# Kernel optimization log

Measured on AMD Instinct MI355X. Metric: run time of the kernel, lower is better.

## Reference

```python
import jax, jax.numpy as jnp
import numpy as np

N = 50000      # nodes
E = 800000     # edges (before self-loops)
DIN = 256      # node_feature_dim
H = 3          # attention heads
C = 64         # hidden channels per head
DOUT = 16      # output_dim
NEG_SLOPE = 0.2


def setup_inputs() -> dict:
    key = jax.random.key(0)
    ks = jax.random.split(key, 12)
    s = 0.05
    return {
        "x": jax.random.normal(ks[0], (N, DIN), dtype=jnp.float32),
        "W1": jax.random.normal(ks[1], (DIN, H * C), dtype=jnp.float32) * s,
        "att_src1": jax.random.normal(ks[2], (H, C), dtype=jnp.float32) * s,
        "att_dst1": jax.random.normal(ks[3], (H, C), dtype=jnp.float32) * s,
        "b1": jnp.zeros((C,), dtype=jnp.float32),
        "W2": jax.random.normal(ks[4], (C, H * C), dtype=jnp.float32) * s,
        "att_src2": jax.random.normal(ks[5], (H, C), dtype=jnp.float32) * s,
        "att_dst2": jax.random.normal(ks[6], (H, C), dtype=jnp.float32) * s,
        "b2": jnp.zeros((C,), dtype=jnp.float32),
        "Wl": jax.random.normal(ks[7], (C, DOUT), dtype=jnp.float32) * s,
        "bl": jnp.zeros((DOUT,), dtype=jnp.float32),
        "edge_index": jax.random.randint(ks[8], (2, E), 0, N, dtype=jnp.int64),
    }


def _gat_layer(x, src, dst, W, att_src, att_dst, bias):
    """PyG GATConv, concat=False (mean over heads), self-loops already in src/dst."""
    n = x.shape[0]
    xw = (x @ W).reshape(n, H, C)                       # [N,H,C]
    a_src = jnp.sum(xw * att_src, axis=-1)              # [N,H]
    a_dst = jnp.sum(xw * att_dst, axis=-1)              # [N,H]
    alpha = jax.nn.leaky_relu(a_src[src] + a_dst[dst], NEG_SLOPE)  # [Etot,H]
    # segment softmax over incoming edges of each dst node
    m = jax.ops.segment_max(alpha, dst, num_segments=n)            # [N,H]
    e = jnp.exp(alpha - m[dst])
    ssum = jax.ops.segment_sum(e, dst, num_segments=n)             # [N,H]
    coef = e / (ssum[dst] + 1e-16)                                 # [Etot,H]
    out = jax.ops.segment_sum(xw[src] * coef[:, :, None], dst, num_segments=n)  # [N,H,C]
    return out.mean(axis=1) + bias                      # [N,C]


def reference(x, W1, att_src1, att_dst1, b1, W2, att_src2, att_dst2, b2, Wl, bl, edge_index):
    n = x.shape[0]
    loops = jnp.arange(n, dtype=edge_index.dtype)       # PyG adds self-loops by default
    src = jnp.concatenate([edge_index[0], loops])
    dst = jnp.concatenate([edge_index[1], loops])
    h = jax.nn.relu(_gat_layer(x, src, dst, W1, att_src1, att_dst1, b1))
    # F.dropout in eval mode is identity
    h = _gat_layer(h, src, dst, W2, att_src2, att_dst2, b2)
    logit = h @ Wl + bl
    return (logit, h)
```

## Files before the change

kernel.cpp:

```cpp
#include <hip/hip_runtime.h>
#include <cmath>

#define NC 192
#define CC 64
#define DOUTK 16

typedef _Float16 f16x8 __attribute__((ext_vector_type(8)));
typedef _Float16 f16x4 __attribute__((ext_vector_type(4)));
typedef float f32x4 __attribute__((ext_vector_type(4)));

__device__ __forceinline__ float lrelu(float x) { return x > 0.f ? x : 0.2f * x; }

__device__ __forceinline__ float wred_sum(float v) {
#pragma unroll
  for (int off = 32; off; off >>= 1) v += __shfl_xor(v, off);
  return v;
}
__device__ __forceinline__ float wred_max(float v) {
#pragma unroll
  for (int off = 32; off; off >>= 1) v = fmaxf(v, __shfl_xor(v, off));
  return v;
}

__global__ void k_hist(const int* __restrict__ dsts, int* __restrict__ deg, int E) {
  int e = blockIdx.x * 256 + threadIdx.x;
  if (e < E) atomicAdd(&deg[dsts[e]], 1);
}

__global__ void k_scan_block(const int* __restrict__ deg, int* __restrict__ rowptr,
                             int* __restrict__ bsum, int Nn) {
  __shared__ int tmp[256];
  int i = blockIdx.x * 256 + threadIdx.x;
  int v = (i < Nn) ? deg[i] : 0;
  tmp[threadIdx.x] = v;
  __syncthreads();
  for (int off = 1; off < 256; off <<= 1) {
    int t = (threadIdx.x >= off) ? tmp[threadIdx.x - off] : 0;
    __syncthreads();
    tmp[threadIdx.x] += t;
    __syncthreads();
  }
  if (i < Nn) rowptr[i] = tmp[threadIdx.x] - v;
  if (threadIdx.x == 255) bsum[blockIdx.x] = tmp[255];
}

__global__ void k_scan_bsum(int* __restrict__ bsum, int B) {
  __shared__ int tmp[256];
  int v = (threadIdx.x < B) ? bsum[threadIdx.x] : 0;
  tmp[threadIdx.x] = v;
  __syncthreads();
  for (int off = 1; off < 256; off <<= 1) {
    int t = (threadIdx.x >= off) ? tmp[threadIdx.x - off] : 0;
    __syncthreads();
    tmp[threadIdx.x] += t;
    __syncthreads();
  }
  if (threadIdx.x < B) bsum[threadIdx.x] = tmp[threadIdx.x] - v;
}

__global__ void k_add_off(int* __restrict__ rowptr, const int* __restrict__ bsum,
                          int* __restrict__ cursor, int Nn) {
  int i = blockIdx.x * 256 + threadIdx.x;
  if (i < Nn) {
    int r = rowptr[i] + bsum[blockIdx.x];
    rowptr[i] = r;
    cursor[i] = r;
  }
}

__global__ void k_scatter(const int* __restrict__ srcs, const int* __restrict__ dsts,
                          int* __restrict__ cursor, int* __restrict__ csr_src, int E) {
  int e = blockIdx.x * 256 + threadIdx.x;
  if (e < E) {
    int d = dsts[e];
    int p = atomicAdd(&cursor[d], 1);
    csr_src[p] = srcs[e];
  }
}

__global__ void k_f2h(const float* __restrict__ in, _Float16* __restrict__ out, int n4) {
  int i = blockIdx.x * 256 + threadIdx.x;
  if (i < n4) {
    float4 v = *(const float4*)(in + (size_t)i * 4);
    f16x4 o;
    o[0] = (_Float16)v.x; o[1] = (_Float16)v.y;
    o[2] = (_Float16)v.z; o[3] = (_Float16)v.w;
    *(f16x4*)(out + (size_t)i * 4) = o;
  }
}

__global__ void k_wT(const float* __restrict__ W, _Float16* __restrict__ WT, int K) {
  int i = blockIdx.x * 256 + threadIdx.x;
  if (i < NC * K) {
    int c = i / K, k = i - c * K;
    WT[i] = (_Float16)W[(size_t)k * NC + c];
  }
}

template<int K>
__global__ __launch_bounds__(256) void k_gemm_mfma_att(
    const _Float16* __restrict__ A, const _Float16* __restrict__ WT,
    const float* __restrict__ att_src, const float* __restrict__ att_dst,
    _Float16* __restrict__ XW, float* __restrict__ asrc, float* __restrict__ adst,
    int M) {
  constexpr int KC = 32;
  constexpr int NCHUNK = K / KC;
  constexpr int AST = 40;
  __shared__ _Float16 As[2][128][AST];
  __shared__ _Float16 Bs[2][192][AST];
  const int tid = threadIdx.x;
  const int lane = tid & 63, wv = tid >> 6;
  const int li = lane & 15, g = lane >> 4;
  const int row0 = blockIdx.x * 128;
  const int srow = tid >> 2, sseg = tid & 3;

  f32x4 acc0[12], acc1[12];
#pragma unroll
  for (int t = 0; t < 12; ++t) {
    acc0[t] = (f32x4){0.f, 0.f, 0.f, 0.f};
    acc1[t] = (f32x4){0.f, 0.f, 0.f, 0.f};
  }

  const int ra0 = (row0 + srow      < M) ? row0 + srow      : M - 1;
  const int ra1 = (row0 + 64 + srow < M) ? row0 + 64 + srow : M - 1;

  f16x8 a_st[2], b_st[3];
  auto stage_load = [&](int c) {
    const size_t ko = (size_t)c * KC + sseg * 8;
    a_st[0] = *(const f16x8*)(A + (size_t)ra0 * K + ko);
    a_st[1] = *(const f16x8*)(A + (size_t)ra1 * K + ko);
    b_st[0] = *(const f16x8*)(WT + (size_t)(srow)       * K + ko);
    b_st[1] = *(const f16x8*)(WT + (size_t)(64 + srow)  * K + ko);
    b_st[2] = *(const f16x8*)(WT + (size_t)(128 + srow) * K + ko);
  };
  auto stage_write = [&](int buf) {
    *(f16x8*)&As[buf][srow][sseg * 8]       = a_st[0];
    *(f16x8*)&As[buf][64 + srow][sseg * 8]  = a_st[1];
    *(f16x8*)&Bs[buf][srow][sseg * 8]       = b_st[0];
    *(f16x8*)&Bs[buf][64 + srow][sseg * 8]  = b_st[1];
    *(f16x8*)&Bs[buf][128 + srow][sseg * 8] = b_st[2];
  };

  stage_load(0);
  stage_write(0);
  __syncthreads();

  for (int c = 0; c < NCHUNK; ++c) {
    const int buf = c & 1;
    if (c + 1 < NCHUNK) stage_load(c + 1);
    f16x8 bf[12];
#pragma unroll
    for (int t = 0; t < 12; ++t) bf[t] = *(const f16x8*)&Bs[buf][t * 16 + li][g * 8];
    f16x8 af0 = *(const f16x8*)&As[buf][wv * 32 + li][g * 8];
    f16x8 af1 = *(const f16x8*)&As[buf][wv * 32 + 16 + li][g * 8];
#pragma unroll
    for (int t = 0; t < 12; ++t) {
      acc0[t] = __builtin_amdgcn_mfma_f32_16x16x32_f16(af0, bf[t], acc0[t], 0, 0, 0);
      acc1[t] = __builtin_amdgcn_mfma_f32_16x16x32_f16(af1, bf[t], acc1[t], 0, 0, 0);
    }
    if (c + 1 < NCHUNK) stage_write((c + 1) & 1);
    __syncthreads();
  }

  float avs[12], avd[12];
#pragma unroll
  for (int t = 0; t < 12; ++t) {
    avs[t] = att_src[t * 16 + li];
    avd[t] = att_dst[t * 16 + li];
  }
#pragma unroll
  for (int mt = 0; mt < 2; ++mt) {
    const f32x4* acc = mt ? acc1 : acc0;
    const int rbase = row0 + wv * 32 + mt * 16 + g * 4;
#pragma unroll
    for (int r = 0; r < 4; ++r) {
      const int row = rbase + r;
      const bool ok = row < M;
#pragma unroll
      for (int t = 0; t < 12; ++t)
        if (ok) XW[(size_t)row * NC + t * 16 + li] = (_Float16)acc[t][r];
#pragma unroll
      for (int h = 0; h < 3; ++h) {
        float s = acc[4*h][r]*avs[4*h] + acc[4*h+1][r]*avs[4*h+1] +
                  acc[4*h+2][r]*avs[4*h+2] + acc[4*h+3][r]*avs[4*h+3];
        float d = acc[4*h][r]*avd[4*h] + acc[4*h+1][r]*avd[4*h+1] +
                  acc[4*h+2][r]*avd[4*h+2] + acc[4*h+3][r]*avd[4*h+3];
#pragma unroll
        for (int off = 8; off; off >>= 1) {
          s += __shfl_xor(s, off);
          d += __shfl_xor(d, off);
        }
        if (ok && li == 0) {
          asrc[row * 3 + h] = s;
          adst[row * 3 + h] = d;
        }
      }
    }
  }
}

template<bool RELU, typename OutT>
__global__ __launch_bounds__(256) void k_aggregate(
    const _Float16* __restrict__ xw, const float* __restrict__ asrc,
    const float* __restrict__ adst, const int* __restrict__ rowptr,
    const int* __restrict__ deg, const int* __restrict__ csr_src,
    const float* __restrict__ bias, OutT* __restrict__ out, int Nn) {
  int wid = threadIdx.x >> 6, lane = threadIdx.x & 63;
  int n = blockIdx.x * 4 + wid;
  if (n >= Nn) return;
  int row = rowptr[n], d = deg[n];
  float ad0 = adst[n * 3], ad1 = adst[n * 3 + 1], ad2 = adst[n * 3 + 2];
  float sa0 = lrelu(asrc[n * 3] + ad0);
  float sa1 = lrelu(asrc[n * 3 + 1] + ad1);
  float sa2 = lrelu(asrc[n * 3 + 2] + ad2);

  float acc0, acc1, acc2, S0, S1, S2;

  if (d <= 64) {
    int s = 0;
    float al0 = -INFINITY, al1 = -INFINITY, al2 = -INFINITY;
    if (lane < d) {
      s = csr_src[row + lane];
      al0 = lrelu(asrc[s * 3] + ad0);
      al1 = lrelu(asrc[s * 3 + 1] + ad1);
      al2 = lrelu(asrc[s * 3 + 2] + ad2);
    }
    float m0 = fmaxf(wred_max(al0), sa0);
    float m1 = fmaxf(wred_max(al1), sa1);
    float m2 = fmaxf(wred_max(al2), sa2);
    float w0 = __expf(al0 - m0);
    float w1 = __expf(al1 - m1);
    float w2 = __expf(al2 - m2);
    float e0 = __expf(sa0 - m0), e1 = __expf(sa1 - m1), e2 = __expf(sa2 - m2);
    S0 = wred_sum(w0) + e0 + 1e-16f;
    S1 = wred_sum(w1) + e1 + 1e-16f;
    S2 = wred_sum(w2) + e2 + 1e-16f;
    const _Float16* xrs = xw + (size_t)n * NC;
    acc0 = e0 * (float)xrs[lane];
    acc1 = e1 * (float)xrs[64 + lane];
    acc2 = e2 * (float)xrs[128 + lane];
    for (int e = 0; e < d; ++e) {
      int se = __shfl(s, e);
      float we0 = __shfl(w0, e), we1 = __shfl(w1, e), we2 = __shfl(w2, e);
      const _Float16* xr = xw + (size_t)se * NC;
      acc0 += we0 * (float)xr[lane];
      acc1 += we1 * (float)xr[64 + lane];
      acc2 += we2 * (float)xr[128 + lane];
    }
  } else {
    float m0 = sa0, m1 = sa1, m2 = sa2;
    for (int e = lane; e < d; e += 64) {
      int s = csr_src[row + e];
      m0 = fmaxf(m0, lrelu(asrc[s * 3] + ad0));
      m1 = fmaxf(m1, lrelu(asrc[s * 3 + 1] + ad1));
      m2 = fmaxf(m2, lrelu(asrc[s * 3 + 2] + ad2));
    }
    m0 = wred_max(m0); m1 = wred_max(m1); m2 = wred_max(m2);
    float p0 = 0.f, p1 = 0.f, p2 = 0.f;
    for (int e = lane; e < d; e += 64) {
      int s = csr_src[row + e];
      p0 += __expf(lrelu(asrc[s * 3] + ad0) - m0);
      p1 += __expf(lrelu(asrc[s * 3 + 1] + ad1) - m1);
      p2 += __expf(lrelu(asrc[s * 3 + 2] + ad2) - m2);
    }
    S0 = wred_sum(p0) + __expf(sa0 - m0) + 1e-16f;
    S1 = wred_sum(p1) + __expf(sa1 - m1) + 1e-16f;
    S2 = wred_sum(p2) + __expf(sa2 - m2) + 1e-16f;
    const _Float16* xrs = xw + (size_t)n * NC;
    acc0 = __expf(sa0 - m0) * (float)xrs[lane];
    acc1 = __expf(sa1 - m1) * (float)xrs[64 + lane];
    acc2 = __expf(sa2 - m2) * (float)xrs[128 + lane];
    for (int e = 0; e < d; ++e) {
      int s = csr_src[row + e];
      float we0 = __expf(lrelu(asrc[s * 3] + ad0) - m0);
      float we1 = __expf(lrelu(asrc[s * 3 + 1] + ad1) - m1);
      float we2 = __expf(lrelu(asrc[s * 3 + 2] + ad2) - m2);
      const _Float16* xr = xw + (size_t)s * NC;
      acc0 += we0 * (float)xr[lane];
      acc1 += we1 * (float)xr[64 + lane];
      acc2 += we2 * (float)xr[128 + lane];
    }
  }

  float o = (acc0 / S0 + acc1 / S1 + acc2 / S2) * (1.f / 3.f) + bias[lane];
  out[(size_t)n * CC + lane] = (OutT)(RELU ? fmaxf(o, 0.f) : o);
}

__global__ void k_logit(const float* __restrict__ h, const float* __restrict__ Wl,
                        const float* __restrict__ bl, float* __restrict__ out, int Nn) {
  __shared__ float wl_s[CC * DOUTK];
  __shared__ float hrow[4][CC];
  int tid = threadIdx.x;
  for (int i = tid; i < CC * DOUTK; i += 256) wl_s[i] = Wl[i];
  int wid = tid >> 6, lane = tid & 63;
  int n = blockIdx.x * 4 + wid;
  if (n < Nn) hrow[wid][lane] = h[(size_t)n * CC + lane];
  __syncthreads();
  if (n < Nn && lane < DOUTK) {
    float acc = bl[lane];
#pragma unroll
    for (int c = 0; c < CC; ++c) acc += hrow[wid][c] * wl_s[c * DOUTK + lane];
    out[(size_t)n * DOUTK + lane] = acc;
  }
}

extern "C" void kernel_launch(void* const* d_in, const int* in_sizes, int n_in,
                              void* d_out, int out_size, void* d_ws, size_t ws_size,
                              hipStream_t stream) {
  const float* x   = (const float*)d_in[0];
  const float* W1  = (const float*)d_in[1];
  const float* as1 = (const float*)d_in[2];
  const float* ad1 = (const float*)d_in[3];
  const float* b1  = (const float*)d_in[4];
  const float* W2  = (const float*)d_in[5];
  const float* as2 = (const float*)d_in[6];
  const float* ad2 = (const float*)d_in[7];
  const float* b2  = (const float*)d_in[8];
  const float* Wl  = (const float*)d_in[9];
  const float* bl  = (const float*)d_in[10];
  const int* edges = (const int*)d_in[11];

  const int Nn = in_sizes[0] / 256;
  const int E  = in_sizes[11] / 2;
  const int* srcs = edges;
  const int* dsts = edges + E;

  float* out_logit = (float*)d_out;
  float* out_h     = (float*)d_out + (size_t)Nn * DOUTK;

  char* p = (char*)d_ws;
  auto alloc = [&](size_t bytes) {
    char* r = p;
    p += (bytes + 255) & ~(size_t)255;
    return r;
  };
  _Float16* xw   = (_Float16*)alloc((size_t)Nn * NC * 2);
  _Float16* xh   = (_Float16*)alloc((size_t)Nn * 256 * 2);
  _Float16* h1h  = (_Float16*)alloc((size_t)Nn * CC * 2);
  _Float16* wT1  = (_Float16*)alloc((size_t)NC * 256 * 2);
  _Float16* wT2  = (_Float16*)alloc((size_t)NC * CC * 2);
  float* asrc    = (float*)alloc((size_t)Nn * 3 * 4);
  float* adst    = (float*)alloc((size_t)Nn * 3 * 4);
  int* deg       = (int*)alloc((size_t)Nn * 4);
  int* rowptr    = (int*)alloc((size_t)Nn * 4);
  int* cursor    = (int*)alloc((size_t)Nn * 4);
  int* bsum      = (int*)alloc(256 * 4);
  int* csr_src   = (int*)alloc((size_t)E * 4);

  const int nB = (Nn + 255) / 256;
  const int eB = (E + 255) / 256;
  const int gB = (Nn + 127) / 128;
  const int aB = (Nn + 3) / 4;

  hipMemsetAsync(deg, 0, (size_t)Nn * 4, stream);
  k_hist<<<eB, 256, 0, stream>>>(dsts, deg, E);
  k_scan_block<<<nB, 256, 0, stream>>>(deg, rowptr, bsum, Nn);
  k_scan_bsum<<<1, 256, 0, stream>>>(bsum, nB);
  k_add_off<<<nB, 256, 0, stream>>>(rowptr, bsum, cursor, Nn);
  k_scatter<<<eB, 256, 0, stream>>>(srcs, dsts, cursor, csr_src, E);

  const int nx4 = Nn * 256 / 4;
  k_f2h<<<(nx4 + 255) / 256, 256, 0, stream>>>(x, xh, nx4);
  k_wT<<<(NC * 256 + 255) / 256, 256, 0, stream>>>(W1, wT1, 256);
  k_wT<<<(NC * CC + 255) / 256, 256, 0, stream>>>(W2, wT2, CC);

  k_gemm_mfma_att<256><<<gB, 256, 0, stream>>>(xh, wT1, as1, ad1, xw, asrc, adst, Nn);
  k_aggregate<true, _Float16><<<aB, 256, 0, stream>>>(xw, asrc, adst, rowptr, deg,
                                                      csr_src, b1, h1h, Nn);

  k_gemm_mfma_att<64><<<gB, 256, 0, stream>>>(h1h, wT2, as2, ad2, xw, asrc, adst, Nn);
  k_aggregate<false, float><<<aB, 256, 0, stream>>>(xw, asrc, adst, rowptr, deg,
                                                    csr_src, b2, out_h, Nn);

  k_logit<<<aB, 256, 0, stream>>>(out_h, Wl, bl, out_logit, Nn);
}
```

Measured before the change: 405.0 us.

## Restructure aggregate fast path: LDS-staged coefficients and 4-wide f16 gathers per head

In the low-degree path of the aggregation kernel, the normalized softmax coefficients (folding in 1/S and the 1/3 head mean) and source indices are now staged in shared memory. The gather is remapped so 48 lanes each load 4 contiguous halves with f16x4 loads instead of three scalar halves per lane. Per-head partial sums are combined with shuffles, and 16 lanes write vectorized outputs. This cuts per-edge shuffles and scalar loads and widens memory transactions, at the cost of a block-wide barrier, idle lanes 48-63 during the gather, and extra LDS traffic.

```diff
diff --git a/kernel.cpp b/kernel.cpp
--- a/kernel.cpp
+++ b/kernel.cpp
@@ -205,25 +205,35 @@
     const float* __restrict__ adst, const int* __restrict__ rowptr,
     const int* __restrict__ deg, const int* __restrict__ csr_src,
     const float* __restrict__ bias, OutT* __restrict__ out, int Nn) {
-  int wid = threadIdx.x >> 6, lane = threadIdx.x & 63;
-  int n = blockIdx.x * 4 + wid;
-  if (n >= Nn) return;
-  int row = rowptr[n], d = deg[n];
-  float ad0 = adst[n * 3], ad1 = adst[n * 3 + 1], ad2 = adst[n * 3 + 2];
-  float sa0 = lrelu(asrc[n * 3] + ad0);
-  float sa1 = lrelu(asrc[n * 3 + 1] + ad1);
-  float sa2 = lrelu(asrc[n * 3 + 2] + ad2);
-
-  float acc0, acc1, acc2, S0, S1, S2;
-
-  if (d <= 64) {
+  __shared__ float coef_lds[4 * 3 * 72];
+  __shared__ int src_lds[4 * 72];
+  const int wid = threadIdx.x >> 6, lane = threadIdx.x & 63;
+  const int n = blockIdx.x * 4 + wid;
+  const bool valid = (n < Nn);
+
+  int row = 0, d = 0;
+  float ad0 = 0, ad1 = 0, ad2 = 0, sa0 = 0, sa1 = 0, sa2 = 0;
+  bool fast = true;
+  if (valid) {
+    row = rowptr[n]; d = deg[n];
+    float3 adv = *(const float3*)(adst + 3 * n);
+    float3 asv = *(const float3*)(asrc + 3 * n);
+    ad0 = adv.x; ad1 = adv.y; ad2 = adv.z;
+    sa0 = lrelu(asv.x + ad0);
+    sa1 = lrelu(asv.y + ad1);
+    sa2 = lrelu(asv.z + ad2);
+    fast = (d <= 64);
+  }
+
+  if (valid && fast) {
     int s = 0;
     float al0 = -INFINITY, al1 = -INFINITY, al2 = -INFINITY;
     if (lane < d) {
       s = csr_src[row + lane];
-      al0 = lrelu(asrc[s * 3] + ad0);
-      al1 = lrelu(asrc[s * 3 + 1] + ad1);
-      al2 = lrelu(asrc[s * 3 + 2] + ad2);
+      float3 av = *(const float3*)(asrc + 3 * s);
+      al0 = lrelu(av.x + ad0);
+      al1 = lrelu(av.y + ad1);
+      al2 = lrelu(av.z + ad2);
     }
     float m0 = fmaxf(wred_max(al0), sa0);
     float m1 = fmaxf(wred_max(al1), sa1);
@@ -231,21 +241,89 @@
     float w0 = __expf(al0 - m0);
     float w1 = __expf(al1 - m1);
     float w2 = __expf(al2 - m2);
-    float e0 = __expf(sa0 - m0), e1 = __expf(sa1 - m1), e2 = __expf(sa2 - m2);
-    S0 = wred_sum(w0) + e0 + 1e-16f;
-    S1 = wred_sum(w1) + e1 + 1e-16f;
-    S2 = wred_sum(w2) + e2 + 1e-16f;
-    const _Float16* xrs = xw + (size_t)n * NC;
-    acc0 = e0 * (float)xrs[lane];
-    acc1 = e1 * (float)xrs[64 + lane];
-    acc2 = e2 * (float)xrs[128 + lane];
-    for (int e = 0; e < d; ++e) {
-      int se = __shfl(s, e);
-      float we0 = __shfl(w0, e), we1 = __shfl(w1, e), we2 = __shfl(w2, e);
-      const _Float16* xr = xw + (size_t)se * NC;
-      acc0 += we0 * (float)xr[lane];
-      acc1 += we1 * (float)xr[64 + lane];
-      acc2 += we2 * (float)xr[128 + lane];
+    float es0 = __expf(sa0 - m0), es1 = __expf(sa1 - m1), es2 = __expf(sa2 - m2);
+    float S0 = wred_sum(w0) + es0 + 1e-16f;
+    float S1 = wred_sum(w1) + es1 + 1e-16f;
+    float S2 = wred_sum(w2) + es2 + 1e-16f;
+    float r0 = 1.f / (3.f * S0), r1 = 1.f / (3.f * S1), r2 = 1.f / (3.f * S2);
+    const int cb = wid * 3 * 72;
+    if (lane < d) {
+      coef_lds[cb + lane]       = w0 * r0;
+      coef_lds[cb + 72 + lane]  = w1 * r1;
+      coef_lds[cb + 144 + lane] = w2 * r2;
+      src_lds[wid * 72 + lane] = s;
+    }
+    if (lane == 0) {
+      coef_lds[cb + d]       = es0 * r0;
+      coef_lds[cb + 72 + d]  = es1 * r1;
+      coef_lds[cb + 144 + d] = es2 * r2;
+      src_lds[wid * 72 + d] = n;
+    }
+  }
+  __syncthreads();
+
+  if (!valid) return;
+
+  if (fast) {
+    const int dd = d + 1;
+    float a0 = 0.f, a1 = 0.f, a2 = 0.f, a3 = 0.f;
+    const int h = (lane < 48) ? (lane >> 4) : 2;
+    const int c4 = (lane & 15) * 4;
+    const int coff = h * 64 + c4;
+    const int cbh = (wid * 3 + h) * 72;
+    if (lane < 48) {
+      for (int e = 0; e < dd; e += 4) {
+        int4 s4 = *(const int4*)&src_lds[wid * 72 + e];
+        {
+          float c = coef_lds[cbh + e];
+          f16x4 v = *(const f16x4*)(xw + (size_t)s4.x * NC + coff);
+          a0 += c * (float)v[0]; a1 += c * (float)v[1];
+          a2 += c * (float)v[2]; a3 += c * (float)v[3];
+        }
+        if (e + 1 < dd) {
+          float c = coef_lds[cbh + e + 1];
+          f16x4 v = *(const f16x4*)(xw + (size_t)s4.y * NC + coff);
+          a0 += c * (float)v[0]; a1 += c * (float)v[1];
+          a2 += c * (float)v[2]; a3 += c * (float)v[3];
+        }
+        if (e + 2 < dd) {
+          float c = coef_lds[cbh + e + 2];
+          f16x4 v = *(const f16x4*)(xw + (size_t)s4.z * NC + coff);
+          a0 += c * (float)v[0]; a1 += c * (float)v[1];
+          a2 += c * (float)v[2]; a3 += c * (float)v[3];
+        }
+        if (e + 3 < dd) {
+          float c = coef_lds[cbh + e + 3];
+          f16x4 v = *(const f16x4*)(xw + (size_t)s4.w * NC + coff);
+          a0 += c * (float)v[0]; a1 += c * (float)v[1];
+          a2 += c * (float)v[2]; a3 += c * (float)v[3];
+        }
+      }
+    }
+    const int lb = lane & 15;
+    float b0 = __shfl(a0, lb + 16), c0 = __shfl(a0, lb + 32);
+    float b1 = __shfl(a1, lb + 16), c1 = __shfl(a1, lb + 32);
+    float b2 = __shfl(a2, lb + 16), c2 = __shfl(a2, lb + 32);
+    float b3 = __shfl(a3, lb + 16), c3 = __shfl(a3, lb + 32);
+    if (lane < 16) {
+      float4 bv = *(const float4*)&bias[lb * 4];
+      float o0 = a0 + b0 + c0 + bv.x;
+      float o1 = a1 + b1 + c1 + bv.y;
+      float o2 = a2 + b2 + c2 + bv.z;
+      float o3 = a3 + b3 + c3 + bv.w;
+      if (RELU) {
+        o0 = fmaxf(o0, 0.f); o1 = fmaxf(o1, 0.f);
+        o2 = fmaxf(o2, 0.f); o3 = fmaxf(o3, 0.f);
+      }
+      if constexpr (sizeof(OutT) == 2) {
+        f16x4 ov;
+        ov[0] = (_Float16)o0; ov[1] = (_Float16)o1;
+        ov[2] = (_Float16)o2; ov[3] = (_Float16)o3;
+        *(f16x4*)(out + (size_t)n * CC + lb * 4) = ov;
+      } else {
+        float4 ov = make_float4(o0, o1, o2, o3);
+        *(float4*)((float*)out + (size_t)n * CC + lb * 4) = ov;
+      }
     }
   } else {
     float m0 = sa0, m1 = sa1, m2 = sa2;
@@ -263,13 +341,13 @@
       p1 += __expf(lrelu(asrc[s * 3 + 1] + ad1) - m1);
       p2 += __expf(lrelu(asrc[s * 3 + 2] + ad2) - m2);
     }
-    S0 = wred_sum(p0) + __expf(sa0 - m0) + 1e-16f;
-    S1 = wred_sum(p1) + __expf(sa1 - m1) + 1e-16f;
-    S2 = wred_sum(p2) + __expf(sa2 - m2) + 1e-16f;
+    float S0 = wred_sum(p0) + __expf(sa0 - m0) + 1e-16f;
+    float S1 = wred_sum(p1) + __expf(sa1 - m1) + 1e-16f;
+    float S2 = wred_sum(p2) + __expf(sa2 - m2) + 1e-16f;
     const _Float16* xrs = xw + (size_t)n * NC;
-    acc0 = __expf(sa0 - m0) * (float)xrs[lane];
-    acc1 = __expf(sa1 - m1) * (float)xrs[64 + lane];
-    acc2 = __expf(sa2 - m2) * (float)xrs[128 + lane];
+    float acc0 = __expf(sa0 - m0) * (float)xrs[lane];
+    float acc1 = __expf(sa1 - m1) * (float)xrs[64 + lane];
+    float acc2 = __expf(sa2 - m2) * (float)xrs[128 + lane];
     for (int e = 0; e < d; ++e) {
       int s = csr_src[row + e];
       float we0 = __expf(lrelu(asrc[s * 3] + ad0) - m0);
@@ -280,10 +358,9 @@
       acc1 += we1 * (float)xr[64 + lane];
       acc2 += we2 * (float)xr[128 + lane];
     }
-  }
-
-  float o = (acc0 / S0 + acc1 / S1 + acc2 / S2) * (1.f / 3.f) + bias[lane];
-  out[(size_t)n * CC + lane] = (OutT)(RELU ? fmaxf(o, 0.f) : o);
+    float o = (acc0 / S0 + acc1 / S1 + acc2 / S2) * (1.f / 3.f) + bias[lane];
+    out[(size_t)n * CC + lane] = (OutT)(RELU ? fmaxf(o, 0.f) : o);
+  }
 }
 
 __global__ void k_logit(const float* __restrict__ h, const float* __restrict__ Wl,
```

After: 411.3 us. Within noise of the previous version (+1.6%).

## Aggregate two nodes per wavefront with LDS-staged coefficients and vectorized gathers

Applied to the files above, without the earlier changes.

Restructures the GAT aggregation so each 64-lane wavefront handles two destination nodes, one per half-wave. It computes the softmax coefficients per half, stages the normalized coefficients and source indices in LDS, and then gathers neighbor features as f16x4 vectors with 48 active lanes, four edges at a time. Partial sums are folded across lanes with shuffles. The aim is fewer wasted lanes for low-degree nodes (average degree about 17) and better memory-level parallelism, at the cost of padded edge iterations, idle lanes, and a duplicated slow path for high-degree nodes.

```diff
diff --git a/kernel.cpp b/kernel.cpp
--- a/kernel.cpp
+++ b/kernel.cpp
@@ -19,6 +19,16 @@
 __device__ __forceinline__ float wred_max(float v) {
 #pragma unroll
   for (int off = 32; off; off >>= 1) v = fmaxf(v, __shfl_xor(v, off));
+  return v;
+}
+__device__ __forceinline__ float h32_sum(float v) {
+#pragma unroll
+  for (int off = 16; off; off >>= 1) v += __shfl_xor(v, off);
+  return v;
+}
+__device__ __forceinline__ float h32_max(float v) {
+#pragma unroll
+  for (int off = 16; off; off >>= 1) v = fmaxf(v, __shfl_xor(v, off));
   return v;
 }
 
@@ -205,85 +215,202 @@
     const float* __restrict__ adst, const int* __restrict__ rowptr,
     const int* __restrict__ deg, const int* __restrict__ csr_src,
     const float* __restrict__ bias, OutT* __restrict__ out, int Nn) {
-  int wid = threadIdx.x >> 6, lane = threadIdx.x & 63;
-  int n = blockIdx.x * 4 + wid;
-  if (n >= Nn) return;
-  int row = rowptr[n], d = deg[n];
-  float ad0 = adst[n * 3], ad1 = adst[n * 3 + 1], ad2 = adst[n * 3 + 2];
-  float sa0 = lrelu(asrc[n * 3] + ad0);
-  float sa1 = lrelu(asrc[n * 3 + 1] + ad1);
-  float sa2 = lrelu(asrc[n * 3 + 2] + ad2);
-
-  float acc0, acc1, acc2, S0, S1, S2;
-
-  if (d <= 64) {
+  __shared__ float coef_lds[4][2][3][40];
+  __shared__ int   src_lds[4][2][40];
+  const int wid = threadIdx.x >> 6, lane = threadIdx.x & 63;
+  const int hf = lane >> 5, lh = lane & 31;
+  const int nbase = blockIdx.x * 8 + wid * 2;
+  const int n0 = nbase + hf;
+  const bool v0 = (n0 < Nn);
+
+  int row = 0, d = 0;
+  float ad0 = 0, ad1 = 0, ad2 = 0, sa0 = 0, sa1 = 0, sa2 = 0;
+  if (v0) {
+    row = rowptr[n0]; d = deg[n0];
+    float3 adv = *(const float3*)(adst + 3 * n0);
+    float3 asv = *(const float3*)(asrc + 3 * n0);
+    ad0 = adv.x; ad1 = adv.y; ad2 = adv.z;
+    sa0 = lrelu(asv.x + ad0);
+    sa1 = lrelu(asv.y + ad1);
+    sa2 = lrelu(asv.z + ad2);
+  }
+
+  if (__all(d <= 32)) {
     int s = 0;
     float al0 = -INFINITY, al1 = -INFINITY, al2 = -INFINITY;
-    if (lane < d) {
-      s = csr_src[row + lane];
-      al0 = lrelu(asrc[s * 3] + ad0);
-      al1 = lrelu(asrc[s * 3 + 1] + ad1);
-      al2 = lrelu(asrc[s * 3 + 2] + ad2);
-    }
-    float m0 = fmaxf(wred_max(al0), sa0);
-    float m1 = fmaxf(wred_max(al1), sa1);
-    float m2 = fmaxf(wred_max(al2), sa2);
+    const bool haveE = v0 && (lh < d);
+    if (haveE) {
+      s = csr_src[row + lh];
+      float3 av = *(const float3*)(asrc + 3 * s);
+      al0 = lrelu(av.x + ad0);
+      al1 = lrelu(av.y + ad1);
+      al2 = lrelu(av.z + ad2);
+    }
+    float m0 = fmaxf(h32_max(al0), sa0);
+    float m1 = fmaxf(h32_max(al1), sa1);
+    float m2 = fmaxf(h32_max(al2), sa2);
     float w0 = __expf(al0 - m0);
     float w1 = __expf(al1 - m1);
     float w2 = __expf(al2 - m2);
-    float e0 = __expf(sa0 - m0), e1 = __expf(sa1 - m1), e2 = __expf(sa2 - m2);
-    S0 = wred_sum(w0) + e0 + 1e-16f;
-    S1 = wred_sum(w1) + e1 + 1e-16f;
-    S2 = wred_sum(w2) + e2 + 1e-16f;
-    const _Float16* xrs = xw + (size_t)n * NC;
-    acc0 = e0 * (float)xrs[lane];
-    acc1 = e1 * (float)xrs[64 + lane];
-    acc2 = e2 * (float)xrs[128 + lane];
-    for (int e = 0; e < d; ++e) {
-      int se = __shfl(s, e);
-      float we0 = __shfl(w0, e), we1 = __shfl(w1, e), we2 = __shfl(w2, e);
-      const _Float16* xr = xw + (size_t)se * NC;
-      acc0 += we0 * (float)xr[lane];
-      acc1 += we1 * (float)xr[64 + lane];
-      acc2 += we2 * (float)xr[128 + lane];
+    float es0 = __expf(sa0 - m0), es1 = __expf(sa1 - m1), es2 = __expf(sa2 - m2);
+    float S0 = h32_sum(w0) + es0 + 1e-16f;
+    float S1 = h32_sum(w1) + es1 + 1e-16f;
+    float S2 = h32_sum(w2) + es2 + 1e-16f;
+    float r0 = 1.f / (3.f * S0), r1 = 1.f / (3.f * S1), r2 = 1.f / (3.f * S2);
+
+    const int nsafe = v0 ? n0 : 0;
+    coef_lds[wid][hf][0][lh] = 0.f;
+    coef_lds[wid][hf][1][lh] = 0.f;
+    coef_lds[wid][hf][2][lh] = 0.f;
+    src_lds[wid][hf][lh] = nsafe;
+    if (lh < 8) {
+      coef_lds[wid][hf][0][32 + lh] = 0.f;
+      coef_lds[wid][hf][1][32 + lh] = 0.f;
+      coef_lds[wid][hf][2][32 + lh] = 0.f;
+      src_lds[wid][hf][32 + lh] = nsafe;
+    }
+    if (v0 && lh == 0) {
+      coef_lds[wid][hf][0][d] = es0 * r0;
+      coef_lds[wid][hf][1][d] = es1 * r1;
+      coef_lds[wid][hf][2][d] = es2 * r2;
+      src_lds[wid][hf][d] = n0;
+    }
+    if (haveE) {
+      coef_lds[wid][hf][0][lh] = w0 * r0;
+      coef_lds[wid][hf][1][lh] = w1 * r1;
+      coef_lds[wid][hf][2][lh] = w2 * r2;
+      src_lds[wid][hf][lh] = s;
+    }
+
+    const int dA = __shfl(d, 0), dB = __shfl(d, 32);
+    const int ddm = (((dA > dB ? dA : dB) + 1) + 3) & ~3;
+
+    float aA0 = 0, aA1 = 0, aA2 = 0, aA3 = 0;
+    float aB0 = 0, aB1 = 0, aB2 = 0, aB3 = 0;
+    const int h = (lane < 48) ? (lane >> 4) : 2;
+    const int coff = h * 64 + (lane & 15) * 4;
+    if (lane < 48) {
+      const float* cA = &coef_lds[wid][0][h][0];
+      const float* cB = &coef_lds[wid][1][h][0];
+      const int* sAp = &src_lds[wid][0][0];
+      const int* sBp = &src_lds[wid][1][0];
+      for (int e = 0; e < ddm; e += 4) {
+        int4 s4a = *(const int4*)&sAp[e];
+        int4 s4b = *(const int4*)&sBp[e];
+        f16x4 va0 = *(const f16x4*)(xw + (size_t)s4a.x * NC + coff);
+        f16x4 va1 = *(const f16x4*)(xw + (size_t)s4a.y * NC + coff);
+        f16x4 va2 = *(const f16x4*)(xw + (size_t)s4a.z * NC + coff);
+        f16x4 va3 = *(const f16x4*)(xw + (size_t)s4a.w * NC + coff);
+        f16x4 vb0 = *(const f16x4*)(xw + (size_t)s4b.x * NC + coff);
+        f16x4 vb1 = *(const f16x4*)(xw + (size_t)s4b.y * NC + coff);
+        f16x4 vb2 = *(const f16x4*)(xw + (size_t)s4b.z * NC + coff);
+        f16x4 vb3 = *(const f16x4*)(xw + (size_t)s4b.w * NC + coff);
+        float ca0 = cA[e], ca1 = cA[e + 1], ca2 = cA[e + 2], ca3 = cA[e + 3];
+        float cb0 = cB[e], cb1 = cB[e + 1], cb2 = cB[e + 2], cb3 = cB[e + 3];
+        aA0 += ca0 * (float)va0[0]; aA1 += ca0 * (float)va0[1];
+        aA2 += ca0 * (float)va0[2]; aA3 += ca0 * (float)va0[3];
+        aA0 += ca1 * (float)va1[0]; aA1 += ca1 * (float)va1[1];
+        aA2 += ca1 * (float)va1[2]; aA3 += ca1 * (float)va1[3];
+        aA0 += ca2 * (float)va2[0]; aA1 += ca2 * (float)va2[1];
+        aA2 += ca2 * (float)va2[2]; aA3 += ca2 * (float)va2[3];
+        aA0 += ca3 * (float)va3[0]; aA1 += ca3 * (float)va3[1];
+        aA2 += ca3 * (float)va3[2]; aA3 += ca3 * (float)va3[3];
+        aB0 += cb0 * (float)vb0[0]; aB1 += cb0 * (float)vb0[1];
+        aB2 += cb0 * (float)vb0[2]; aB3 += cb0 * (float)vb0[3];
+        aB0 += cb1 * (float)vb1[0]; aB1 += cb1 * (float)vb1[1];
+        aB2 += cb1 * (float)vb1[2]; aB3 += cb1 * (float)vb1[3];
+        aB0 += cb2 * (float)vb2[0]; aB1 += cb2 * (float)vb2[1];
+        aB2 += cb2 * (float)vb2[2]; aB3 += cb2 * (float)vb2[3];
+        aB0 += cb3 * (float)vb3[0]; aB1 += cb3 * (float)vb3[1];
+        aB2 += cb3 * (float)vb3[2]; aB3 += cb3 * (float)vb3[3];
+      }
+    }
+
+    const int lb = lane & 15;
+#define FOLD3(a) ((a) + __shfl((a), lb + 16) + __shfl((a), lb + 32))
+    float oA0 = FOLD3(aA0), oA1 = FOLD3(aA1), oA2 = FOLD3(aA2), oA3 = FOLD3(aA3);
+    float oB0 = FOLD3(aB0), oB1 = FOLD3(aB1), oB2 = FOLD3(aB2), oB3 = FOLD3(aB3);
+#undef FOLD3
+    if (lane < 16) {
+      float4 bv = *(const float4*)&bias[lb * 4];
+      if (nbase < Nn) {
+        float p0 = oA0 + bv.x, p1 = oA1 + bv.y, p2 = oA2 + bv.z, p3 = oA3 + bv.w;
+        if (RELU) {
+          p0 = fmaxf(p0, 0.f); p1 = fmaxf(p1, 0.f);
+          p2 = fmaxf(p2, 0.f); p3 = fmaxf(p3, 0.f);
+        }
+        if constexpr (sizeof(OutT) == 2) {
+          f16x4 ov; ov[0] = (_Float16)p0; ov[1] = (_Float16)p1;
+          ov[2] = (_Float16)p2; ov[3] = (_Float16)p3;
+          *(f16x4*)(out + (size_t)nbase * CC + lb * 4) = ov;
+        } else {
+          *(float4*)((float*)out + (size_t)nbase * CC + lb * 4) =
+              make_float4(p0, p1, p2, p3);
+        }
+      }
+      if (nbase + 1 < Nn) {
+        float p0 = oB0 + bv.x, p1 = oB1 + bv.y, p2 = oB2 + bv.z, p3 = oB3 + bv.w;
+        if (RELU) {
+          p0 = fmaxf(p0, 0.f); p1 = fmaxf(p1, 0.f);
+          p2 = fmaxf(p2, 0.f); p3 = fmaxf(p3, 0.f);
+        }
+        if constexpr (sizeof(OutT) == 2) {
+          f16x4 ov; ov[0] = (_Float16)p0; ov[1] = (_Float16)p1;
+          ov[2] = (_Float16)p2; ov[3] = (_Float16)p3;
+          *(f16x4*)(out + (size_t)(nbase + 1) * CC + lb * 4) = ov;
+        } else {
+          *(float4*)((float*)out + (size_t)(nbase + 1) * CC + lb * 4) =
+              make_float4(p0, p1, p2, p3);
+        }
+      }
     }
   } else {
-    float m0 = sa0, m1 = sa1, m2 = sa2;
-    for (int e = lane; e < d; e += 64) {
-      int s = csr_src[row + e];
-      m0 = fmaxf(m0, lrelu(asrc[s * 3] + ad0));
-      m1 = fmaxf(m1, lrelu(asrc[s * 3 + 1] + ad1));
-      m2 = fmaxf(m2, lrelu(asrc[s * 3 + 2] + ad2));
-    }
-    m0 = wred_max(m0); m1 = wred_max(m1); m2 = wred_max(m2);
-    float p0 = 0.f, p1 = 0.f, p2 = 0.f;
-    for (int e = lane; e < d; e += 64) {
-      int s = csr_src[row + e];
-      p0 += __expf(lrelu(asrc[s * 3] + ad0) - m0);
-      p1 += __expf(lrelu(asrc[s * 3 + 1] + ad1) - m1);
-      p2 += __expf(lrelu(asrc[s * 3 + 2] + ad2) - m2);
-    }
-    S0 = wred_sum(p0) + __expf(sa0 - m0) + 1e-16f;
-    S1 = wred_sum(p1) + __expf(sa1 - m1) + 1e-16f;
-    S2 = wred_sum(p2) + __expf(sa2 - m2) + 1e-16f;
-    const _Float16* xrs = xw + (size_t)n * NC;
-    acc0 = __expf(sa0 - m0) * (float)xrs[lane];
-    acc1 = __expf(sa1 - m1) * (float)xrs[64 + lane];
-    acc2 = __expf(sa2 - m2) * (float)xrs[128 + lane];
-    for (int e = 0; e < d; ++e) {
-      int s = csr_src[row + e];
-      float we0 = __expf(lrelu(asrc[s * 3] + ad0) - m0);
-      float we1 = __expf(lrelu(asrc[s * 3 + 1] + ad1) - m1);
-      float we2 = __expf(lrelu(asrc[s * 3 + 2] + ad2) - m2);
-      const _Float16* xr = xw + (size_t)s * NC;
-      acc0 += we0 * (float)xr[lane];
-      acc1 += we1 * (float)xr[64 + lane];
-      acc2 += we2 * (float)xr[128 + lane];
-    }
-  }
-
-  float o = (acc0 / S0 + acc1 / S1 + acc2 / S2) * (1.f / 3.f) + bias[lane];
-  out[(size_t)n * CC + lane] = (OutT)(RELU ? fmaxf(o, 0.f) : o);
+    for (int k2 = 0; k2 < 2; ++k2) {
+      const int nx = nbase + k2;
+      if (nx >= Nn) continue;
+      const int rowx = rowptr[nx], dx = deg[nx];
+      float3 adv = *(const float3*)(adst + 3 * nx);
+      float3 asv = *(const float3*)(asrc + 3 * nx);
+      const float bd0 = adv.x, bd1 = adv.y, bd2 = adv.z;
+      const float ss0 = lrelu(asv.x + bd0);
+      const float ss1 = lrelu(asv.y + bd1);
+      const float ss2 = lrelu(asv.z + bd2);
+      float m0 = ss0, m1 = ss1, m2 = ss2;
+      for (int e = lane; e < dx; e += 64) {
+        int s = csr_src[rowx + e];
+        m0 = fmaxf(m0, lrelu(asrc[s * 3] + bd0));
+        m1 = fmaxf(m1, lrelu(asrc[s * 3 + 1] + bd1));
+        m2 = fmaxf(m2, lrelu(asrc[s * 3 + 2] + bd2));
+      }
+      m0 = wred_max(m0); m1 = wred_max(m1); m2 = wred_max(m2);
+      float p0 = 0.f, p1 = 0.f, p2 = 0.f;
+      for (int e = lane; e < dx; e += 64) {
+        int s = csr_src[rowx + e];
+        p0 += __expf(lrelu(asrc[s * 3] + bd0) - m0);
+        p1 += __expf(lrelu(asrc[s * 3 + 1] + bd1) - m1);
+        p2 += __expf(lrelu(asrc[s * 3 + 2] + bd2) - m2);
+      }
+      float S0 = wred_sum(p0) + __expf(ss0 - m0) + 1e-16f;
+      float S1 = wred_sum(p1) + __expf(ss1 - m1) + 1e-16f;
+      float S2 = wred_sum(p2) + __expf(ss2 - m2) + 1e-16f;
+      const _Float16* xrs = xw + (size_t)nx * NC;
+      float acc0 = __expf(ss0 - m0) * (float)xrs[lane];
+      float acc1 = __expf(ss1 - m1) * (float)xrs[64 + lane];
+      float acc2 = __expf(ss2 - m2) * (float)xrs[128 + lane];
+      for (int e = 0; e < dx; ++e) {
+        int s = csr_src[rowx + e];
+        float we0 = __expf(lrelu(asrc[s * 3] + bd0) - m0);
+        float we1 = __expf(lrelu(asrc[s * 3 + 1] + bd1) - m1);
+        float we2 = __expf(lrelu(asrc[s * 3 + 2] + bd2) - m2);
+        const _Float16* xr = xw + (size_t)s * NC;
+        acc0 += we0 * (float)xr[lane];
+        acc1 += we1 * (float)xr[64 + lane];
+        acc2 += we2 * (float)xr[128 + lane];
+      }
+      float o = (acc0 / S0 + acc1 / S1 + acc2 / S2) * (1.f / 3.f) + bias[lane];
+      out[(size_t)nx * CC + lane] = (OutT)(RELU ? fmaxf(o, 0.f) : o);
+    }
+  }
 }
 
 __global__ void k_logit(const float* __restrict__ h, const float* __restrict__ Wl,
@@ -350,7 +477,8 @@
   const int nB = (Nn + 255) / 256;
   const int eB = (E + 255) / 256;
   const int gB = (Nn + 127) / 128;
-  const int aB = (Nn + 3) / 4;
+  const int aB = (Nn + 7) / 8;
+  const int lB = (Nn + 3) / 4;
 
   hipMemsetAsync(deg, 0, (size_t)Nn * 4, stream);
   k_hist<<<eB, 256, 0, stream>>>(dsts, deg, E);
@@ -372,5 +500,5 @@
   k_aggregate<false, float><<<aB, 256, 0, stream>>>(xw, asrc, adst, rowptr, deg,
                                                     csr_src, b2, out_h, Nn);
 
-  k_logit<<<aB, 256, 0, stream>>>(out_h, Wl, bl, out_logit, Nn);
-}
+  k_logit<<<lB, 256, 0, stream>>>(out_h, Wl, bl, out_logit, Nn);
+}
```

Result: faster. 385.8 us (-4.7%).
